# Kernel tuning notes

Hardware: AMD Instinct MI355X
Metric: run time of the kernel (lower is better)

Reference implementation:

```python
import jax, jax.numpy as jnp
import numpy as np

NUM_HEADS = 16
THRESHOLD = 4e-4  # < 1/S so every softmax row keeps >=1 entry (classical path of grover_search_filter)


def setup_inputs() -> dict:
    key = jax.random.key(0)
    k0, k1, k2 = jax.random.split(key, 3)
    B, S, E = 4, 1024, 1024
    x = jax.random.normal(k0, (B, S, E), dtype=jnp.float32)
    Wqkv = jax.random.normal(k1, (3 * E, E), dtype=jnp.float32) * 0.02
    bqkv = jnp.zeros((3 * E,), dtype=jnp.float32)
    Wproj = jax.random.normal(k2, (E, E), dtype=jnp.float32) * 0.02
    bproj = jnp.zeros((E,), dtype=jnp.float32)
    return {"x": x, "Wqkv": Wqkv, "bqkv": bqkv, "Wproj": Wproj, "bproj": bproj}


def reference(x, Wqkv, bqkv, Wproj, bproj):
    B, S, E = x.shape
    H = NUM_HEADS
    D = E // H
    scale = D ** -0.5
    # qkv projection -> (3, B, H, S, D), matching torch permute(2,0,3,1,4)
    qkv = (x @ Wqkv.T + bqkv).reshape(B, S, 3, H, D).transpose(2, 0, 3, 1, 4)
    q, k, v = qkv[0], qkv[1], qkv[2]
    attn_logits = jnp.einsum("bhqd,bhkd->bhqk", q, k) * scale  # [B,H,S,S]
    attn_probs = jax.nn.softmax(attn_logits, axis=-1)
    # grover_search_filter: seq_len > 2**max_qubits -> classical threshold mask
    selected = attn_probs > THRESHOLD
    filtered_logits = jnp.where(selected, attn_logits, -jnp.inf)
    filtered_attn = jax.nn.softmax(filtered_logits, axis=-1)
    # dropout is identity in eval mode
    out = jnp.einsum("bhqk,bhkd->bhqd", filtered_attn, v)
    out = out.transpose(0, 2, 1, 3).reshape(B, S, E)
    out = out @ Wproj.T + bproj
    return out, filtered_attn
```

## Files before the change

### kernel.cpp

```cpp
#include <hip/hip_runtime.h>
#include <hip/hip_bf16.h>
#include <cstdint>


#define BB 4
#define SS 1024
#define EE 1024
#define HH 16
#define DD 64

typedef __attribute__((ext_vector_type(8))) short bf16x8;
typedef __attribute__((ext_vector_type(4))) float f32x4;

__global__ __launch_bounds__(256) void split_f32(
    const float* __restrict__ in, __hip_bfloat16* __restrict__ hi,
    __hip_bfloat16* __restrict__ lo, int n4) {
  int i = blockIdx.x * 256 + threadIdx.x;
  if (i >= n4) return;
  float4 v = ((const float4*)in)[i];
  float vv[4] = {v.x, v.y, v.z, v.w};
  __hip_bfloat16 h[4], l[4];
#pragma unroll
  for (int j = 0; j < 4; ++j) {
    h[j] = __float2bfloat16(vv[j]);
    l[j] = __float2bfloat16(vv[j] - __bfloat162float(h[j]));
  }
  ((ushort4*)hi)[i] = *(ushort4*)h;
  if (lo) ((ushort4*)lo)[i] = *(ushort4*)l;
}

template <int MODE>
__global__ __launch_bounds__(256) void gemm(
    const __hip_bfloat16* __restrict__ Ah, const __hip_bfloat16* __restrict__ Al,
    const __hip_bfloat16* __restrict__ Bh, const __hip_bfloat16* __restrict__ Bl,
    const float* __restrict__ Af, const float* __restrict__ bias,
    float* __restrict__ oF, __hip_bfloat16* __restrict__ o1,
    __hip_bfloat16* __restrict__ o2, __hip_bfloat16* __restrict__ o3,
    __hip_bfloat16* __restrict__ o4, __hip_bfloat16* __restrict__ o5,
    int M, int N, int K, int lda, int ldb, long long sA, long long sB) {
  constexpr bool SPLIT = (MODE == 0 || MODE == 1);
  constexpr bool AF32  = (MODE == 2);

  const int tid  = threadIdx.x;
  const int lane = tid & 63;
  const int wave = tid >> 6;
  const int wm   = (wave >> 1) * 64;
  const int wn   = (wave & 1) * 64;
  const int quad = lane >> 4;
  const int l15  = lane & 15;
  const int m0   = blockIdx.y * 128;
  const int n0   = blockIdx.x * 128;
  const long long zz = blockIdx.z;

  if (AF32) Af += zz * sA;
  else { Ah += zz * sA; if (SPLIT) Al += zz * sA; }
  Bh += zz * sB;
  if (SPLIT) Bl += zz * sB;

  __shared__ __align__(16) __hip_bfloat16 lds[(SPLIT ? 4 : 2) * 128 * 72];
  __hip_bfloat16* lAh = lds;
  __hip_bfloat16* lAl = SPLIT ? lds + 128 * 72 : nullptr;
  __hip_bfloat16* lBh = lds + (SPLIT ? 2 : 1) * 128 * 72;
  __hip_bfloat16* lBl = SPLIT ? lds + 3 * 128 * 72 : nullptr;

  f32x4 acc[4][4] = {};

  for (int k0 = 0; k0 < K; k0 += 64) {
#pragma unroll
    for (int it = 0; it < 4; ++it) {
      int flat = (it * 256 + tid) * 8;
      int row  = flat >> 6;
      int kk   = flat & 63;
      const bool mok = (m0 + row < M);
      const bool nok = (n0 + row < N);
      if (AF32) {
        float4 f0 = {0, 0, 0, 0}, f1 = {0, 0, 0, 0};
        if (mok) {
          const float* src = Af + (long long)(m0 + row) * lda + k0 + kk;
          f0 = *(const float4*)src;
          f1 = *(const float4*)(src + 4);
        }
        __hip_bfloat16 t[8];
        t[0] = __float2bfloat16(f0.x); t[1] = __float2bfloat16(f0.y);
        t[2] = __float2bfloat16(f0.z); t[3] = __float2bfloat16(f0.w);
        t[4] = __float2bfloat16(f1.x); t[5] = __float2bfloat16(f1.y);
        t[6] = __float2bfloat16(f1.z); t[7] = __float2bfloat16(f1.w);
        *(uint4*)&lAh[row * 72 + kk] = *(uint4*)t;
      } else {
        uint4 va = {0, 0, 0, 0};
        if (mok) va = *(const uint4*)(Ah + (long long)(m0 + row) * lda + k0 + kk);
        *(uint4*)&lAh[row * 72 + kk] = va;
        if (SPLIT) {
          uint4 vl = {0, 0, 0, 0};
          if (mok) vl = *(const uint4*)(Al + (long long)(m0 + row) * lda + k0 + kk);
          *(uint4*)&lAl[row * 72 + kk] = vl;
        }
      }
      uint4 vb = {0, 0, 0, 0};
      if (nok) vb = *(const uint4*)(Bh + (long long)(n0 + row) * ldb + k0 + kk);
      *(uint4*)&lBh[row * 72 + kk] = vb;
      if (SPLIT) {
        uint4 vbl = {0, 0, 0, 0};
        if (nok) vbl = *(const uint4*)(Bl + (long long)(n0 + row) * ldb + k0 + kk);
        *(uint4*)&lBl[row * 72 + kk] = vbl;
      }
    }
    __syncthreads();

#pragma unroll
    for (int ks = 0; ks < 64; ks += 32) {
      bf16x8 ah[4], bh[4], al[4], bl[4];
#pragma unroll
      for (int i = 0; i < 4; ++i) {
        int off = (wm + i * 16 + l15) * 72 + ks + quad * 8;
        ah[i] = *(const bf16x8*)&lAh[off];
        if (SPLIT) al[i] = *(const bf16x8*)&lAl[off];
      }
#pragma unroll
      for (int j = 0; j < 4; ++j) {
        int off = (wn + j * 16 + l15) * 72 + ks + quad * 8;
        bh[j] = *(const bf16x8*)&lBh[off];
        if (SPLIT) bl[j] = *(const bf16x8*)&lBl[off];
      }
#pragma unroll
      for (int i = 0; i < 4; ++i)
#pragma unroll
        for (int j = 0; j < 4; ++j) {
          if (SPLIT) {
            acc[i][j] = __builtin_amdgcn_mfma_f32_16x16x32_bf16(al[i], bh[j], acc[i][j], 0, 0, 0);
            acc[i][j] = __builtin_amdgcn_mfma_f32_16x16x32_bf16(ah[i], bl[j], acc[i][j], 0, 0, 0);
          }
          acc[i][j] = __builtin_amdgcn_mfma_f32_16x16x32_bf16(ah[i], bh[j], acc[i][j], 0, 0, 0);
        }
    }
    __syncthreads();
  }

#pragma unroll
  for (int i = 0; i < 4; ++i) {
#pragma unroll
    for (int j = 0; j < 4; ++j) {
#pragma unroll
      for (int r = 0; r < 4; ++r) {
        int m = m0 + wm + i * 16 + quad * 4 + r;
        int n = n0 + wn + j * 16 + l15;
        float v = acc[i][j][r];
        if (MODE == 0) {
          v += bias[n];
          int c = n >> 10, nn = n & 1023, h = nn >> 6, d = nn & 63;
          int b = m >> 10, s = m & 1023;
          long long idx = (((long long)(b * HH + h) * SS + s) << 6) + d;
          if (c == 0) {
            __hip_bfloat16 hh = __float2bfloat16(v);
            o1[idx] = hh;
            o2[idx] = __float2bfloat16(v - __bfloat162float(hh));
          } else if (c == 1) {
            __hip_bfloat16 hh = __float2bfloat16(v);
            o3[idx] = hh;
            o4[idx] = __float2bfloat16(v - __bfloat162float(hh));
          } else {
            o5[(((long long)(b * HH + h) * DD + d) << 10) + s] = __float2bfloat16(v);
          }
        } else if (MODE == 1) {
          oF[zz * (SS * SS) + (long long)m * SS + n] = v * 0.125f;
        } else if (MODE == 2) {
          if (n < DD) {
            int b = (int)(zz >> 4), h = (int)(zz & 15);
            o1[(((long long)(b * SS + m)) << 10) + h * DD + n] = __float2bfloat16(v);
          }
        } else {
          oF[(long long)m * EE + n] = v + bias[n];
        }
      }
    }
  }
}

__device__ __forceinline__ float qg_max16(float v) {
#pragma unroll
  for (int o = 8; o > 0; o >>= 1) v = fmaxf(v, __shfl_xor(v, o));
  return v;
}
__device__ __forceinline__ float qg_sum16(float v) {
#pragma unroll
  for (int o = 8; o > 0; o >>= 1) v += __shfl_xor(v, o);
  return v;
}

__global__ __launch_bounds__(512, 6) void fused_attn(
    const __hip_bfloat16* __restrict__ qh, const __hip_bfloat16* __restrict__ ql,
    const __hip_bfloat16* __restrict__ kh, const __hip_bfloat16* __restrict__ kl,
    const __hip_bfloat16* __restrict__ vT, float* __restrict__ attn,
    __hip_bfloat16* __restrict__ ao) {
  const int tid  = threadIdx.x;
  const int lane = tid & 63;
  const int wave = tid >> 6;
  const int quad = lane >> 4;
  const int l15  = lane & 15;

  int id = blockIdx.x;
  const int q8 = gridDim.x >> 3;
  id = (id & 7) * q8 + (id >> 3);
  const int bh = id >> 6;
  const int q0 = (id & 63) * 16;

  const int brow = (bh >> 4) * SS;
  const int h    = bh & 15;
  const long long qbase = ((long long)bh * SS + q0) * DD;
  const long long kbase = (long long)bh * SS * DD;
  const long long vbase = (long long)bh * DD * SS;
  const long long abase = ((long long)bh * SS + q0) * SS;

  __shared__ __align__(16) __hip_bfloat16 Pl[16][1032];
  __shared__ float red[3][8][16];
  __shared__ float Obuf[4][16][18];

  bf16x8 aqh0, aqh1, aql0, aql1;
  {
    const __hip_bfloat16* ph = qh + qbase + l15 * DD + quad * 8;
    const __hip_bfloat16* pl = ql + qbase + l15 * DD + quad * 8;
    aqh0 = *(const bf16x8*)(ph);
    aqh1 = *(const bf16x8*)(ph + 32);
    aql0 = *(const bf16x8*)(pl);
    aql1 = *(const bf16x8*)(pl + 32);
  }

  f32x4 acc[8];
  const __hip_bfloat16* pkh0 = kh + kbase + (long long)(wave * 128 + l15) * DD + quad * 8;
  const __hip_bfloat16* pkl0 = kl + kbase + (long long)(wave * 128 + l15) * DD + quad * 8;
#pragma unroll
  for (int nt = 0; nt < 8; ++nt) {
    const __hip_bfloat16* pkh = pkh0 + nt * 16 * DD;
    const __hip_bfloat16* pkl = pkl0 + nt * 16 * DD;
    bf16x8 b0 = *(const bf16x8*)(pkh);
    bf16x8 b1 = *(const bf16x8*)(pkh + 32);
    bf16x8 c0 = *(const bf16x8*)(pkl);
    bf16x8 c1 = *(const bf16x8*)(pkl + 32);
    f32x4 a = {};
    __builtin_amdgcn_s_setprio(1);
    a = __builtin_amdgcn_mfma_f32_16x16x32_bf16(aql0, b0, a, 0, 0, 0);
    a = __builtin_amdgcn_mfma_f32_16x16x32_bf16(aqh0, c0, a, 0, 0, 0);
    a = __builtin_amdgcn_mfma_f32_16x16x32_bf16(aqh0, b0, a, 0, 0, 0);
    a = __builtin_amdgcn_mfma_f32_16x16x32_bf16(aql1, b1, a, 0, 0, 0);
    a = __builtin_amdgcn_mfma_f32_16x16x32_bf16(aqh1, c1, a, 0, 0, 0);
    a = __builtin_amdgcn_mfma_f32_16x16x32_bf16(aqh1, b1, a, 0, 0, 0);
    __builtin_amdgcn_s_setprio(0);
    acc[nt] = a;
  }

#pragma unroll
  for (int nt = 0; nt < 8; ++nt)
#pragma unroll
    for (int r = 0; r < 4; ++r) acc[nt][r] *= 0.125f;

  float mx[4];
#pragma unroll
  for (int r = 0; r < 4; ++r) {
    float mm = acc[0][r];
#pragma unroll
    for (int nt = 1; nt < 8; ++nt) mm = fmaxf(mm, acc[nt][r]);
    mx[r] = qg_max16(mm);
  }
  if (l15 == 0) {
#pragma unroll
    for (int r = 0; r < 4; ++r) red[0][wave][quad * 4 + r] = mx[r];
  }
  __syncthreads();
  float m[4];
#pragma unroll
  for (int r = 0; r < 4; ++r) {
    const int q = quad * 4 + r;
    float a01 = fmaxf(red[0][0][q], red[0][1][q]);
    float a23 = fmaxf(red[0][2][q], red[0][3][q]);
    float a45 = fmaxf(red[0][4][q], red[0][5][q]);
    float a67 = fmaxf(red[0][6][q], red[0][7][q]);
    m[r] = fmaxf(fmaxf(a01, a23), fmaxf(a45, a67));
  }

  float zl[4] = {0.f, 0.f, 0.f, 0.f};
#pragma unroll
  for (int nt = 0; nt < 8; ++nt)
#pragma unroll
    for (int r = 0; r < 4; ++r) {
      float e = expf(acc[nt][r] - m[r]);
      acc[nt][r] = e;
      zl[r] += e;
    }
#pragma unroll
  for (int r = 0; r < 4; ++r) zl[r] = qg_sum16(zl[r]);
  if (l15 == 0) {
#pragma unroll
    for (int r = 0; r < 4; ++r) red[1][wave][quad * 4 + r] = zl[r];
  }
  __syncthreads();
  float c[4];
#pragma unroll
  for (int r = 0; r < 4; ++r) {
    const int q = quad * 4 + r;
    const float Z = ((red[1][0][q] + red[1][1][q]) + (red[1][2][q] + red[1][3][q])) +
                    ((red[1][4][q] + red[1][5][q]) + (red[1][6][q] + red[1][7][q]));
    c[r] = 4e-4f * Z;
  }

  float sl[4] = {0.f, 0.f, 0.f, 0.f};
#pragma unroll
  for (int nt = 0; nt < 8; ++nt)
#pragma unroll
    for (int r = 0; r < 4; ++r)
      if (acc[nt][r] > c[r]) sl[r] += acc[nt][r];
#pragma unroll
  for (int r = 0; r < 4; ++r) sl[r] = qg_sum16(sl[r]);
  if (l15 == 0) {
#pragma unroll
    for (int r = 0; r < 4; ++r) red[2][wave][quad * 4 + r] = sl[r];
  }
  __syncthreads();
  float rinv[4];
#pragma unroll
  for (int r = 0; r < 4; ++r) {
    const int q = quad * 4 + r;
    const float Zs = ((red[2][0][q] + red[2][1][q]) + (red[2][2][q] + red[2][3][q])) +
                     ((red[2][4][q] + red[2][5][q]) + (red[2][6][q] + red[2][7][q]));
    rinv[r] = 1.0f / Zs;
  }

#pragma unroll
  for (int nt = 0; nt < 8; ++nt) {
    const int k = wave * 128 + nt * 16 + l15;
#pragma unroll
    for (int r = 0; r < 4; ++r) {
      const int q = quad * 4 + r;
      const float e = acc[nt][r];
      const float p = (e > c[r]) ? e * rinv[r] : 0.f;
      __builtin_nontemporal_store(p, &attn[abase + (long long)q * SS + k]);
      Pl[q][k] = __float2bfloat16(p);
    }
  }
  __syncthreads();

  const int d0  = (wave & 3) * 16;
  const int kh2 = (wave >> 2) * 512;
  f32x4 o0 = {}, o1 = {};
  const __hip_bfloat16* pv = vT + vbase + (long long)(d0 + l15) * SS + kh2 + quad * 8;
  const __hip_bfloat16* pp = &Pl[l15][kh2] + quad * 8;
#pragma unroll
  for (int ks = 0; ks < 16; ks += 2) {
    bf16x8 a0 = *(const bf16x8*)(pp + ks * 32);
    bf16x8 v0 = *(const bf16x8*)(pv + ks * 32);
    bf16x8 a1 = *(const bf16x8*)(pp + (ks + 1) * 32);
    bf16x8 v1 = *(const bf16x8*)(pv + (ks + 1) * 32);
    __builtin_amdgcn_s_setprio(1);
    o0 = __builtin_amdgcn_mfma_f32_16x16x32_bf16(a0, v0, o0, 0, 0, 0);
    o1 = __builtin_amdgcn_mfma_f32_16x16x32_bf16(a1, v1, o1, 0, 0, 0);
    __builtin_amdgcn_s_setprio(0);
  }
  if (wave >= 4) {
#pragma unroll
    for (int r = 0; r < 4; ++r)
      Obuf[wave & 3][quad * 4 + r][l15] = o0[r] + o1[r];
  }
  __syncthreads();
  if (wave < 4) {
#pragma unroll
    for (int r = 0; r < 4; ++r) {
      const int q = q0 + quad * 4 + r;
      const float v = o0[r] + o1[r] + Obuf[wave][quad * 4 + r][l15];
      ao[((long long)(brow + q)) * EE + h * DD + d0 + l15] = __float2bfloat16(v);
    }
  }
}

extern "C" void kernel_launch(void* const* d_in, const int* in_sizes, int n_in,
                              void* d_out, int out_size, void* d_ws, size_t ws_size,
                              hipStream_t stream) {
  const float* x     = (const float*)d_in[0];
  const float* Wqkv  = (const float*)d_in[1];
  const float* bqkv  = (const float*)d_in[2];
  const float* Wproj = (const float*)d_in[3];
  const float* bproj = (const float*)d_in[4];

  float* out   = (float*)d_out;
  float* attnF = out + (size_t)BB * SS * EE;

  const size_t M1 = 1024 * 1024;
  __hip_bfloat16* w = (__hip_bfloat16*)d_ws;

  if (ws_size >= (size_t)80 * 1024 * 1024) {
    __hip_bfloat16 *xh = w, *xl = xh + 4 * M1;
    __hip_bfloat16 *Wqh = xl + 4 * M1, *Wql = Wqh + 3 * M1, *Wph = Wql + 3 * M1;
    __hip_bfloat16 *qh = Wph + M1, *ql = qh + 4 * M1, *kh = ql + 4 * M1, *kl = kh + 4 * M1;
    __hip_bfloat16 *vT = kl + 4 * M1, *ao = vT + 4 * M1;

    split_f32<<<4096, 256, 0, stream>>>(x, xh, xl, 1024 * 1024);
    split_f32<<<3072, 256, 0, stream>>>(Wqkv, Wqh, Wql, 768 * 1024);
    split_f32<<<1024, 256, 0, stream>>>(Wproj, Wph, nullptr, 256 * 1024);

    gemm<0><<<dim3(24, 32, 1), 256, 0, stream>>>(
        xh, xl, Wqh, Wql, nullptr, bqkv, nullptr, qh, ql, kh, kl, vT,
        4096, 3072, 1024, 1024, 1024, 0LL, 0LL);
    fused_attn<<<dim3(BB * HH * 64), 512, 0, stream>>>(
        qh, ql, kh, kl, vT, attnF, ao);
    gemm<3><<<dim3(8, 32, 1), 256, 0, stream>>>(
        ao, nullptr, Wph, nullptr, nullptr, bproj, out, nullptr, nullptr, nullptr, nullptr, nullptr,
        4096, 1024, 1024, 1024, 1024, 0LL, 0LL);
    return;
  }

  __hip_bfloat16 *Wqh = w, *Wql = Wqh + 3 * M1, *Wph = Wql + 3 * M1;
  __hip_bfloat16 *xh = Wph + M1, *xl = xh + M1;
  __hip_bfloat16 *qh = xl + M1, *ql = qh + M1, *kh = ql + M1, *kl = kh + M1;
  __hip_bfloat16 *vT = kl + M1, *ao = vT + M1;

  split_f32<<<3072, 256, 0, stream>>>(Wqkv, Wqh, Wql, 768 * 1024);
  split_f32<<<1024, 256, 0, stream>>>(Wproj, Wph, nullptr, 256 * 1024);

  for (int b = 0; b < BB; ++b) {
    const float* xb   = x + (size_t)b * SS * EE;
    float* attnb      = attnF + (size_t)b * HH * SS * SS;
    float* outb       = out + (size_t)b * SS * EE;

    split_f32<<<1024, 256, 0, stream>>>(xb, xh, xl, 256 * 1024);
    gemm<0><<<dim3(24, 8, 1), 256, 0, stream>>>(
        xh, xl, Wqh, Wql, nullptr, bqkv, nullptr, qh, ql, kh, kl, vT,
        1024, 3072, 1024, 1024, 1024, 0LL, 0LL);
    fused_attn<<<dim3(HH * 64), 512, 0, stream>>>(
        qh, ql, kh, kl, vT, attnb, ao);
    gemm<3><<<dim3(8, 8, 1), 256, 0, stream>>>(
        ao, nullptr, Wph, nullptr, nullptr, bproj, outb, nullptr, nullptr, nullptr, nullptr, nullptr,
        1024, 1024, 1024, 1024, 1024, 0LL, 0LL);
  }
}
```

Before: 668.9 us.

## Process 32 query rows per attention block to reuse K and V loads

```diff
diff --git a/kernel.cpp b/kernel.cpp
--- a/kernel.cpp
+++ b/kernel.cpp
@@ -151,6 +151,7 @@
           int b = m >> 10, s = m & 1023;
           long long idx = (((long long)(b * HH + h) * SS + s) << 6) + d;
           if (c == 0) {
+            v *= 0.125f;
             __hip_bfloat16 hh = __float2bfloat16(v);
             o1[idx] = hh;
             o2[idx] = __float2bfloat16(v - __bfloat162float(hh));
@@ -187,7 +188,7 @@
   return v;
 }
 
-__global__ __launch_bounds__(512, 6) void fused_attn(
+__global__ __launch_bounds__(512, 4) void fused_attn(
     const __hip_bfloat16* __restrict__ qh, const __hip_bfloat16* __restrict__ ql,
     const __hip_bfloat16* __restrict__ kh, const __hip_bfloat16* __restrict__ kl,
     const __hip_bfloat16* __restrict__ vT, float* __restrict__ attn,
@@ -201,8 +202,8 @@
   int id = blockIdx.x;
   const int q8 = gridDim.x >> 3;
   id = (id & 7) * q8 + (id >> 3);
-  const int bh = id >> 6;
-  const int q0 = (id & 63) * 16;
+  const int bh = id >> 5;
+  const int q0 = (id & 31) * 32;
 
   const int brow = (bh >> 4) * SS;
   const int h    = bh & 15;
@@ -211,117 +212,151 @@
   const long long vbase = (long long)bh * DD * SS;
   const long long abase = ((long long)bh * SS + q0) * SS;
 
-  __shared__ __align__(16) __hip_bfloat16 Pl[16][1032];
-  __shared__ float red[3][8][16];
-  __shared__ float Obuf[4][16][18];
-
-  bf16x8 aqh0, aqh1, aql0, aql1;
-  {
-    const __hip_bfloat16* ph = qh + qbase + l15 * DD + quad * 8;
-    const __hip_bfloat16* pl = ql + qbase + l15 * DD + quad * 8;
-    aqh0 = *(const bf16x8*)(ph);
-    aqh1 = *(const bf16x8*)(ph + 32);
-    aql0 = *(const bf16x8*)(pl);
-    aql1 = *(const bf16x8*)(pl + 32);
-  }
-
-  f32x4 acc[8];
+  __shared__ __align__(16) __hip_bfloat16 Pl[32][1032];
+  __shared__ float red[3][8][32];
+  __shared__ float Obuf[4][32][17];
+
+  bf16x8 aqh0[2], aqh1[2], aql0[2], aql1[2];
+#pragma unroll
+  for (int s = 0; s < 2; ++s) {
+    const __hip_bfloat16* ph = qh + qbase + (s * 16 + l15) * DD + quad * 8;
+    const __hip_bfloat16* pl = ql + qbase + (s * 16 + l15) * DD + quad * 8;
+    aqh0[s] = *(const bf16x8*)(ph);
+    aqh1[s] = *(const bf16x8*)(ph + 32);
+    aql0[s] = *(const bf16x8*)(pl);
+    aql1[s] = *(const bf16x8*)(pl + 32);
+  }
+
+  f32x4 acc0[8], acc1[8];
   const __hip_bfloat16* pkh0 = kh + kbase + (long long)(wave * 128 + l15) * DD + quad * 8;
   const __hip_bfloat16* pkl0 = kl + kbase + (long long)(wave * 128 + l15) * DD + quad * 8;
 #pragma unroll
   for (int nt = 0; nt < 8; ++nt) {
     const __hip_bfloat16* pkh = pkh0 + nt * 16 * DD;
     const __hip_bfloat16* pkl = pkl0 + nt * 16 * DD;
-    bf16x8 b0 = *(const bf16x8*)(pkh);
-    bf16x8 b1 = *(const bf16x8*)(pkh + 32);
-    bf16x8 c0 = *(const bf16x8*)(pkl);
-    bf16x8 c1 = *(const bf16x8*)(pkl + 32);
-    f32x4 a = {};
-    __builtin_amdgcn_s_setprio(1);
-    a = __builtin_amdgcn_mfma_f32_16x16x32_bf16(aql0, b0, a, 0, 0, 0);
-    a = __builtin_amdgcn_mfma_f32_16x16x32_bf16(aqh0, c0, a, 0, 0, 0);
-    a = __builtin_amdgcn_mfma_f32_16x16x32_bf16(aqh0, b0, a, 0, 0, 0);
-    a = __builtin_amdgcn_mfma_f32_16x16x32_bf16(aql1, b1, a, 0, 0, 0);
-    a = __builtin_amdgcn_mfma_f32_16x16x32_bf16(aqh1, c1, a, 0, 0, 0);
-    a = __builtin_amdgcn_mfma_f32_16x16x32_bf16(aqh1, b1, a, 0, 0, 0);
-    __builtin_amdgcn_s_setprio(0);
-    acc[nt] = a;
-  }
-
-#pragma unroll
-  for (int nt = 0; nt < 8; ++nt)
-#pragma unroll
-    for (int r = 0; r < 4; ++r) acc[nt][r] *= 0.125f;
-
-  float mx[4];
-#pragma unroll
-  for (int r = 0; r < 4; ++r) {
-    float mm = acc[0][r];
-#pragma unroll
-    for (int nt = 1; nt < 8; ++nt) mm = fmaxf(mm, acc[nt][r]);
-    mx[r] = qg_max16(mm);
-  }
-  if (l15 == 0) {
-#pragma unroll
-    for (int r = 0; r < 4; ++r) red[0][wave][quad * 4 + r] = mx[r];
+    f32x4 a0 = {}, a1 = {};
+    {
+      bf16x8 b = *(const bf16x8*)(pkh);
+      bf16x8 c = *(const bf16x8*)(pkl);
+      __builtin_amdgcn_s_setprio(1);
+      a0 = __builtin_amdgcn_mfma_f32_16x16x32_bf16(aql0[0], b, a0, 0, 0, 0);
+      a1 = __builtin_amdgcn_mfma_f32_16x16x32_bf16(aql0[1], b, a1, 0, 0, 0);
+      a0 = __builtin_amdgcn_mfma_f32_16x16x32_bf16(aqh0[0], c, a0, 0, 0, 0);
+      a1 = __builtin_amdgcn_mfma_f32_16x16x32_bf16(aqh0[1], c, a1, 0, 0, 0);
+      a0 = __builtin_amdgcn_mfma_f32_16x16x32_bf16(aqh0[0], b, a0, 0, 0, 0);
+      a1 = __builtin_amdgcn_mfma_f32_16x16x32_bf16(aqh0[1], b, a1, 0, 0, 0);
+      __builtin_amdgcn_s_setprio(0);
+    }
+    {
+      bf16x8 b = *(const bf16x8*)(pkh + 32);
+      bf16x8 c = *(const bf16x8*)(pkl + 32);
+      __builtin_amdgcn_s_setprio(1);
+      a0 = __builtin_amdgcn_mfma_f32_16x16x32_bf16(aql1[0], b, a0, 0, 0, 0);
+      a1 = __builtin_amdgcn_mfma_f32_16x16x32_bf16(aql1[1], b, a1, 0, 0, 0);
+      a0 = __builtin_amdgcn_mfma_f32_16x16x32_bf16(aqh1[0], c, a0, 0, 0, 0);
+      a1 = __builtin_amdgcn_mfma_f32_16x16x32_bf16(aqh1[1], c, a1, 0, 0, 0);
+      a0 = __builtin_amdgcn_mfma_f32_16x16x32_bf16(aqh1[0], b, a0, 0, 0, 0);
+      a1 = __builtin_amdgcn_mfma_f32_16x16x32_bf16(aqh1[1], b, a1, 0, 0, 0);
+      __builtin_amdgcn_s_setprio(0);
+    }
+    acc0[nt] = a0;
+    acc1[nt] = a1;
+  }
+
+  {
+    float mx0[4], mx1[4];
+#pragma unroll
+    for (int r = 0; r < 4; ++r) {
+      float a = fmaxf(fmaxf(fmaxf(acc0[0][r], acc0[1][r]), fmaxf(acc0[2][r], acc0[3][r])),
+                      fmaxf(fmaxf(acc0[4][r], acc0[5][r]), fmaxf(acc0[6][r], acc0[7][r])));
+      mx0[r] = qg_max16(a);
+      float b = fmaxf(fmaxf(fmaxf(acc1[0][r], acc1[1][r]), fmaxf(acc1[2][r], acc1[3][r])),
+                      fmaxf(fmaxf(acc1[4][r], acc1[5][r]), fmaxf(acc1[6][r], acc1[7][r])));
+      mx1[r] = qg_max16(b);
+    }
+    if (l15 == 0) {
+#pragma unroll
+      for (int r = 0; r < 4; ++r) {
+        red[0][wave][quad * 4 + r]      = mx0[r];
+        red[0][wave][16 + quad * 4 + r] = mx1[r];
+      }
+    }
   }
   __syncthreads();
-  float m[4];
+  float m0[4], m1[4];
 #pragma unroll
   for (int r = 0; r < 4; ++r) {
     const int q = quad * 4 + r;
-    float a01 = fmaxf(red[0][0][q], red[0][1][q]);
-    float a23 = fmaxf(red[0][2][q], red[0][3][q]);
-    float a45 = fmaxf(red[0][4][q], red[0][5][q]);
-    float a67 = fmaxf(red[0][6][q], red[0][7][q]);
-    m[r] = fmaxf(fmaxf(a01, a23), fmaxf(a45, a67));
-  }
-
-  float zl[4] = {0.f, 0.f, 0.f, 0.f};
-#pragma unroll
-  for (int nt = 0; nt < 8; ++nt)
-#pragma unroll
-    for (int r = 0; r < 4; ++r) {
-      float e = expf(acc[nt][r] - m[r]);
-      acc[nt][r] = e;
-      zl[r] += e;
-    }
-#pragma unroll
-  for (int r = 0; r < 4; ++r) zl[r] = qg_sum16(zl[r]);
-  if (l15 == 0) {
-#pragma unroll
-    for (int r = 0; r < 4; ++r) red[1][wave][quad * 4 + r] = zl[r];
+    m0[r] = fmaxf(fmaxf(fmaxf(red[0][0][q], red[0][1][q]), fmaxf(red[0][2][q], red[0][3][q])),
+                  fmaxf(fmaxf(red[0][4][q], red[0][5][q]), fmaxf(red[0][6][q], red[0][7][q])));
+    m1[r] = fmaxf(fmaxf(fmaxf(red[0][0][16 + q], red[0][1][16 + q]), fmaxf(red[0][2][16 + q], red[0][3][16 + q])),
+                  fmaxf(fmaxf(red[0][4][16 + q], red[0][5][16 + q]), fmaxf(red[0][6][16 + q], red[0][7][16 + q])));
+  }
+
+  {
+    float z0[4] = {0.f, 0.f, 0.f, 0.f}, z1[4] = {0.f, 0.f, 0.f, 0.f};
+#pragma unroll
+    for (int nt = 0; nt < 8; ++nt)
+#pragma unroll
+      for (int r = 0; r < 4; ++r) {
+        float e0 = expf(acc0[nt][r] - m0[r]);
+        acc0[nt][r] = e0; z0[r] += e0;
+        float e1 = expf(acc1[nt][r] - m1[r]);
+        acc1[nt][r] = e1; z1[r] += e1;
+      }
+#pragma unroll
+    for (int r = 0; r < 4; ++r) { z0[r] = qg_sum16(z0[r]); z1[r] = qg_sum16(z1[r]); }
+    if (l15 == 0) {
+#pragma unroll
+      for (int r = 0; r < 4; ++r) {
+        red[1][wave][quad * 4 + r]      = z0[r];
+        red[1][wave][16 + quad * 4 + r] = z1[r];
+      }
+    }
   }
   __syncthreads();
-  float c[4];
+  float c0[4], c1[4];
 #pragma unroll
   for (int r = 0; r < 4; ++r) {
     const int q = quad * 4 + r;
-    const float Z = ((red[1][0][q] + red[1][1][q]) + (red[1][2][q] + red[1][3][q])) +
-                    ((red[1][4][q] + red[1][5][q]) + (red[1][6][q] + red[1][7][q]));
-    c[r] = 4e-4f * Z;
-  }
-
-  float sl[4] = {0.f, 0.f, 0.f, 0.f};
-#pragma unroll
-  for (int nt = 0; nt < 8; ++nt)
-#pragma unroll
-    for (int r = 0; r < 4; ++r)
-      if (acc[nt][r] > c[r]) sl[r] += acc[nt][r];
-#pragma unroll
-  for (int r = 0; r < 4; ++r) sl[r] = qg_sum16(sl[r]);
-  if (l15 == 0) {
-#pragma unroll
-    for (int r = 0; r < 4; ++r) red[2][wave][quad * 4 + r] = sl[r];
+    const float Z0 = ((red[1][0][q] + red[1][1][q]) + (red[1][2][q] + red[1][3][q])) +
+                     ((red[1][4][q] + red[1][5][q]) + (red[1][6][q] + red[1][7][q]));
+    const float Z1 = ((red[1][0][16 + q] + red[1][1][16 + q]) + (red[1][2][16 + q] + red[1][3][16 + q])) +
+                     ((red[1][4][16 + q] + red[1][5][16 + q]) + (red[1][6][16 + q] + red[1][7][16 + q]));
+    c0[r] = 4e-4f * Z0;
+    c1[r] = 4e-4f * Z1;
+  }
+
+  {
+    float s0[4] = {0.f, 0.f, 0.f, 0.f}, s1[4] = {0.f, 0.f, 0.f, 0.f};
+#pragma unroll
+    for (int nt = 0; nt < 8; ++nt)
+#pragma unroll
+      for (int r = 0; r < 4; ++r) {
+        if (acc0[nt][r] > c0[r]) s0[r] += acc0[nt][r];
+        if (acc1[nt][r] > c1[r]) s1[r] += acc1[nt][r];
+      }
+#pragma unroll
+    for (int r = 0; r < 4; ++r) { s0[r] = qg_sum16(s0[r]); s1[r] = qg_sum16(s1[r]); }
+    if (l15 == 0) {
+#pragma unroll
+      for (int r = 0; r < 4; ++r) {
+        red[2][wave][quad * 4 + r]      = s0[r];
+        red[2][wave][16 + quad * 4 + r] = s1[r];
+      }
+    }
   }
   __syncthreads();
-  float rinv[4];
+  float rinv0[4], rinv1[4];
 #pragma unroll
   for (int r = 0; r < 4; ++r) {
     const int q = quad * 4 + r;
-    const float Zs = ((red[2][0][q] + red[2][1][q]) + (red[2][2][q] + red[2][3][q])) +
-                     ((red[2][4][q] + red[2][5][q]) + (red[2][6][q] + red[2][7][q]));
-    rinv[r] = 1.0f / Zs;
+    const float Zs0 = ((red[2][0][q] + red[2][1][q]) + (red[2][2][q] + red[2][3][q])) +
+                      ((red[2][4][q] + red[2][5][q]) + (red[2][6][q] + red[2][7][q]));
+    const float Zs1 = ((red[2][0][16 + q] + red[2][1][16 + q]) + (red[2][2][16 + q] + red[2][3][16 + q])) +
+                      ((red[2][4][16 + q] + red[2][5][16 + q]) + (red[2][6][16 + q] + red[2][7][16 + q]));
+    rinv0[r] = 1.0f / Zs0;
+    rinv1[r] = 1.0f / Zs1;
   }
 
 #pragma unroll
@@ -330,42 +365,60 @@
 #pragma unroll
     for (int r = 0; r < 4; ++r) {
       const int q = quad * 4 + r;
-      const float e = acc[nt][r];
-      const float p = (e > c[r]) ? e * rinv[r] : 0.f;
-      __builtin_nontemporal_store(p, &attn[abase + (long long)q * SS + k]);
-      Pl[q][k] = __float2bfloat16(p);
+      const float e0 = acc0[nt][r];
+      const float p0 = (e0 > c0[r]) ? e0 * rinv0[r] : 0.f;
+      attn[abase + (long long)q * SS + k] = p0;
+      Pl[q][k] = __float2bfloat16(p0);
+      const float e1 = acc1[nt][r];
+      const float p1 = (e1 > c1[r]) ? e1 * rinv1[r] : 0.f;
+      attn[abase + (long long)(16 + q) * SS + k] = p1;
+      Pl[16 + q][k] = __float2bfloat16(p1);
     }
   }
   __syncthreads();
 
   const int d0  = (wave & 3) * 16;
   const int kh2 = (wave >> 2) * 512;
-  f32x4 o0 = {}, o1 = {};
-  const __hip_bfloat16* pv = vT + vbase + (long long)(d0 + l15) * SS + kh2 + quad * 8;
-  const __hip_bfloat16* pp = &Pl[l15][kh2] + quad * 8;
+  f32x4 oA0 = {}, oA1 = {}, oB0 = {}, oB1 = {};
+  const __hip_bfloat16* pv  = vT + vbase + (long long)(d0 + l15) * SS + kh2 + quad * 8;
+  const __hip_bfloat16* pp0 = &Pl[l15][kh2] + quad * 8;
+  const __hip_bfloat16* pp1 = &Pl[16 + l15][kh2] + quad * 8;
 #pragma unroll
   for (int ks = 0; ks < 16; ks += 2) {
-    bf16x8 a0 = *(const bf16x8*)(pp + ks * 32);
-    bf16x8 v0 = *(const bf16x8*)(pv + ks * 32);
-    bf16x8 a1 = *(const bf16x8*)(pp + (ks + 1) * 32);
-    bf16x8 v1 = *(const bf16x8*)(pv + (ks + 1) * 32);
+    bf16x8 v0  = *(const bf16x8*)(pv + ks * 32);
+    bf16x8 v1  = *(const bf16x8*)(pv + (ks + 1) * 32);
+    bf16x8 a00 = *(const bf16x8*)(pp0 + ks * 32);
+    bf16x8 a01 = *(const bf16x8*)(pp0 + (ks + 1) * 32);
+    bf16x8 a10 = *(const bf16x8*)(pp1 + ks * 32);
+    bf16x8 a11 = *(const bf16x8*)(pp1 + (ks + 1) * 32);
     __builtin_amdgcn_s_setprio(1);
-    o0 = __builtin_amdgcn_mfma_f32_16x16x32_bf16(a0, v0, o0, 0, 0, 0);
-    o1 = __builtin_amdgcn_mfma_f32_16x16x32_bf16(a1, v1, o1, 0, 0, 0);
+    oA0 = __builtin_amdgcn_mfma_f32_16x16x32_bf16(a00, v0, oA0, 0, 0, 0);
+    oB0 = __builtin_amdgcn_mfma_f32_16x16x32_bf16(a10, v0, oB0, 0, 0, 0);
+    oA1 = __builtin_amdgcn_mfma_f32_16x16x32_bf16(a01, v1, oA1, 0, 0, 0);
+    oB1 = __builtin_amdgcn_mfma_f32_16x16x32_bf16(a11, v1, oB1, 0, 0, 0);
     __builtin_amdgcn_s_setprio(0);
   }
+  float oS0[4], oS1[4];
+#pragma unroll
+  for (int r = 0; r < 4; ++r) { oS0[r] = oA0[r] + oA1[r]; oS1[r] = oB0[r] + oB1[r]; }
+
   if (wave >= 4) {
 #pragma unroll
-    for (int r = 0; r < 4; ++r)
-      Obuf[wave & 3][quad * 4 + r][l15] = o0[r] + o1[r];
+    for (int r = 0; r < 4; ++r) {
+      Obuf[wave & 3][quad * 4 + r][l15]      = oS0[r];
+      Obuf[wave & 3][16 + quad * 4 + r][l15] = oS1[r];
+    }
   }
   __syncthreads();
   if (wave < 4) {
 #pragma unroll
     for (int r = 0; r < 4; ++r) {
-      const int q = q0 + quad * 4 + r;
-      const float v = o0[r] + o1[r] + Obuf[wave][quad * 4 + r][l15];
-      ao[((long long)(brow + q)) * EE + h * DD + d0 + l15] = __float2bfloat16(v);
+      const int qA = q0 + quad * 4 + r;
+      const int qB = qA + 16;
+      const float vA = oS0[r] + Obuf[wave][quad * 4 + r][l15];
+      const float vB = oS1[r] + Obuf[wave][16 + quad * 4 + r][l15];
+      ao[((long long)(brow + qA)) * EE + h * DD + d0 + l15] = __float2bfloat16(vA);
+      ao[((long long)(brow + qB)) * EE + h * DD + d0 + l15] = __float2bfloat16(vB);
     }
   }
 }
@@ -398,7 +451,7 @@
     gemm<0><<<dim3(24, 32, 1), 256, 0, stream>>>(
         xh, xl, Wqh, Wql, nullptr, bqkv, nullptr, qh, ql, kh, kl, vT,
         4096, 3072, 1024, 1024, 1024, 0LL, 0LL);
-    fused_attn<<<dim3(BB * HH * 64), 512, 0, stream>>>(
+    fused_attn<<<dim3(BB * HH * 32), 512, 0, stream>>>(
         qh, ql, kh, kl, vT, attnF, ao);
     gemm<3><<<dim3(8, 32, 1), 256, 0, stream>>>(
         ao, nullptr, Wph, nullptr, nullptr, bproj, out, nullptr, nullptr, nullptr, nullptr, nullptr,
@@ -423,7 +476,7 @@
     gemm<0><<<dim3(24, 8, 1), 256, 0, stream>>>(
         xh, xl, Wqh, Wql, nullptr, bqkv, nullptr, qh, ql, kh, kl, vT,
         1024, 3072, 1024, 1024, 1024, 0LL, 0LL);
-    fused_attn<<<dim3(HH * 64), 512, 0, stream>>>(
+    fused_attn<<<dim3(HH * 32), 512, 0, stream>>>(
         qh, ql, kh, kl, vT, attnb, ao);
     gemm<3><<<dim3(8, 8, 1), 256, 0, stream>>>(
         ao, nullptr, Wph, nullptr, nullptr, bproj, outb, nullptr, nullptr, nullptr, nullptr, nullptr,
```

Measured after the change: 670.4 us. No clear change (+0.2%).
